# Kernel optimization log

Hardware: AMD Instinct MI355X
Metric: run time of the kernel (lower is better)

## Reference

```python
import jax, jax.numpy as jnp
import numpy as np

NEG_INF = -1e18  # fp32 masking constant used by the original module


def setup_inputs() -> dict:
    key0 = jax.random.key(0)
    kq, kk, kv, km, ke = jax.random.split(key0, 5)
    B, L, H, C = 2, 2048, 16, 64
    query = jax.random.normal(kq, (B, L, H, C), dtype=jnp.float32)
    key = jax.random.normal(kk, (B, L, H, C), dtype=jnp.float32)
    value = jax.random.normal(kv, (B, L, H, C), dtype=jnp.float32)
    mask = jax.random.randint(km, (B, L, L), 0, 2).astype(jnp.bool_)
    edge_scores = jax.random.normal(ke, (1, H, L, L), dtype=jnp.float32)
    return {"query": query, "key": key, "value": value, "mask": mask,
            "edge_scores": edge_scores}


def _masked_softmax(att_score, mask):
    # mask: True -> keep, False -> masked. Fill with -1e18 (fp32 path),
    # softmax, then multiply by mask (post-softmax zeroing), as in original.
    s = jnp.where(mask, att_score, NEG_INF)
    w = jax.nn.softmax(s, axis=-1)
    return w * mask.astype(w.dtype)


def reference(query, key, value, mask, edge_scores):
    # layout 'NTK': query/key/value (B, L, H, C); mask (B, Lq, Lm)
    scale = jnp.sqrt(jnp.asarray(query.shape[-1], dtype=query.dtype))
    # scores: (B, H, Lq, Lm)
    scores = jnp.einsum('binc,bjnc->bnij', query, key)
    scores = scores + edge_scores
    attn_weights = _masked_softmax(scores / scale, mask[:, None, :, :])
    # dropout rate is 0.0 -> identity
    # context: (B, Lq, H, Cv) -> (B, Lq, H*Cv)
    context = jnp.einsum('bnij,bjnc->binc', attn_weights, value)
    B, Lq = context.shape[0], context.shape[1]
    context_vec = context.reshape(B, Lq, -1)
    return (context_vec, scores, attn_weights)
```

## Files before the change

kernel.cpp:

```cpp
#include <hip/hip_runtime.h>


typedef __attribute__((ext_vector_type(8))) short bf16x8;
typedef __attribute__((ext_vector_type(4))) float f32x4;
typedef __attribute__((ext_vector_type(4))) int   i32x4;

#define LQ 2048
#define NH 16
#define CD 64

__device__ inline short f2bf(float x) {
    union { float f; unsigned u; } v; v.f = x;
    unsigned r = v.u + 0x7FFFu + ((v.u >> 16) & 1u);
    return (short)(r >> 16);
}

__device__ inline bf16x8 pack8(f32x4 a, f32x4 b) {
    bf16x8 r;
    r[0] = f2bf(a[0]); r[1] = f2bf(a[1]); r[2] = f2bf(a[2]); r[3] = f2bf(a[3]);
    r[4] = f2bf(b[0]); r[5] = f2bf(b[1]); r[6] = f2bf(b[2]); r[7] = f2bf(b[3]);
    return r;
}

__device__ inline void lds_barrier() {
    asm volatile("s_waitcnt lgkmcnt(0)" ::: "memory");
    __builtin_amdgcn_s_barrier();
}

__global__ __launch_bounds__(256, 4)
void k_attn(const float* __restrict__ q, const float* __restrict__ kk,
            const float* __restrict__ v, const int* __restrict__ mask,
            const float* __restrict__ edge,
            float* __restrict__ sc, float* __restrict__ attn,
            float* __restrict__ ctx)
{
    __shared__ short KsD[2][64][66];
    __shared__ short Vt[64][66];
    __shared__ short Wt[4][16][66];

    const int flat = blockIdx.x;
    const int L = (flat & 7) * 128 + (flat >> 3);
    const int z = L >> 5;
    const int i0 = (L & 31) * 64;
    const int b = z & 1, h = z >> 1;

    const int tid = threadIdx.x;
    const int r = tid >> 2, seg = (tid & 3) * 16;
    const int wave = tid >> 6, lane = tid & 63;
    const int quad = lane >> 4, mm = lane & 15;

    const int gi = i0 + wave * 16 + mm;
    const float* qp = q + ((size_t)((b * LQ + gi) * NH + h)) * CD;
    bf16x8 qa0 = pack8(*(const f32x4*)(qp + quad * 8), *(const f32x4*)(qp + quad * 8 + 4));
    bf16x8 qa1 = pack8(*(const f32x4*)(qp + 32 + quad * 8), *(const f32x4*)(qp + 32 + quad * 8 + 4));

    const float* erow = edge + ((size_t)(h * LQ + gi)) * LQ;
    const int*   mrow = mask + ((size_t)(b * LQ + gi)) * LQ;
    const size_t srow = ((size_t)((b * NH + h) * LQ + gi)) * LQ;

    const float* kbase = kk + ((size_t)((b * LQ + r) * NH + h)) * CD + seg;
    const float* vbase = v  + ((size_t)((b * LQ + r) * NH + h)) * CD + seg;
    const size_t kstep = (size_t)64 * NH * CD;

    f32x4 ev[4]; i32x4 mv[4];
    #pragma unroll
    for (int jt = 0; jt < 4; ++jt) {
        ev[jt] = *(const f32x4*)(erow + jt * 16 + quad * 4);
        mv[jt] = *(const i32x4*)(mrow + jt * 16 + quad * 4);
    }

    f32x4 kr[4];
    #pragma unroll
    for (int u = 0; u < 4; ++u) kr[u] = ((const f32x4*)kbase)[u];
    #pragma unroll
    for (int u = 0; u < 4; ++u)
        *(short4*)&KsD[0][r][seg + u * 4] =
            make_short4(f2bf(kr[u][0]), f2bf(kr[u][1]), f2bf(kr[u][2]), f2bf(kr[u][3]));
    #pragma unroll
    for (int u = 0; u < 4; ++u) kr[u] = ((const f32x4*)(kbase + kstep))[u];
    lds_barrier();

    float lacc = 0.f;
    for (int jb = 0; jb < 32; ++jb) {
        const int j0 = jb * 64;
        const int cur = jb & 1;
        if (jb < 31) {
            #pragma unroll
            for (int u = 0; u < 4; ++u)
                *(short4*)&KsD[cur ^ 1][r][seg + u * 4] =
                    make_short4(f2bf(kr[u][0]), f2bf(kr[u][1]), f2bf(kr[u][2]), f2bf(kr[u][3]));
            if (jb < 30) {
                const float* kp = kbase + kstep * (jb + 2);
                #pragma unroll
                for (int u = 0; u < 4; ++u) kr[u] = ((const f32x4*)kp)[u];
            }
        }
        f32x4 acc[4];
        #pragma unroll
        for (int jt = 0; jt < 4; ++jt) {
            bf16x8 k0 = *(const bf16x8*)&KsD[cur][jt * 16 + mm][quad * 8];
            bf16x8 k1 = *(const bf16x8*)&KsD[cur][jt * 16 + mm][32 + quad * 8];
            f32x4 a = {0.f, 0.f, 0.f, 0.f};
            a = __builtin_amdgcn_mfma_f32_16x16x32_bf16(k0, qa0, a, 0, 0, 0);
            a = __builtin_amdgcn_mfma_f32_16x16x32_bf16(k1, qa1, a, 0, 0, 0);
            acc[jt] = a;
        }
        #pragma unroll
        for (int jt = 0; jt < 4; ++jt) {
            f32x4 s4 = acc[jt] + ev[jt];
            *(f32x4*)(sc + srow + j0 + jt * 16 + quad * 4) = s4;
            lacc += (mv[jt][0] ? __expf(s4[0] * 0.125f) : 0.f)
                  + (mv[jt][1] ? __expf(s4[1] * 0.125f) : 0.f)
                  + (mv[jt][2] ? __expf(s4[2] * 0.125f) : 0.f)
                  + (mv[jt][3] ? __expf(s4[3] * 0.125f) : 0.f);
        }
        if (jb < 31) {
            #pragma unroll
            for (int jt = 0; jt < 4; ++jt) {
                ev[jt] = *(const f32x4*)(erow + j0 + 64 + jt * 16 + quad * 4);
                mv[jt] = *(const i32x4*)(mrow + j0 + 64 + jt * 16 + quad * 4);
            }
        }
        lds_barrier();
    }

    lacc += __shfl_xor(lacc, 16, 64);
    lacc += __shfl_xor(lacc, 32, 64);
    const float inv = (lacc > 0.f) ? 1.f / lacc : 0.f;

    f32x4 vr[4];
    #pragma unroll
    for (int u = 0; u < 4; ++u) { kr[u] = ((const f32x4*)kbase)[u]; vr[u] = ((const f32x4*)vbase)[u]; }
    #pragma unroll
    for (int jt = 0; jt < 4; ++jt) {
        ev[jt] = *(const f32x4*)(erow + jt * 16 + quad * 4);
        mv[jt] = *(const i32x4*)(mrow + jt * 16 + quad * 4);
    }
    f32x4 cacc[4] = { {0,0,0,0}, {0,0,0,0}, {0,0,0,0}, {0,0,0,0} };

    for (int jb = 0; jb < 32; ++jb) {
        const int j0 = jb * 64;
        #pragma unroll
        for (int u = 0; u < 4; ++u) {
            *(short4*)&KsD[0][r][seg + u * 4] =
                make_short4(f2bf(kr[u][0]), f2bf(kr[u][1]), f2bf(kr[u][2]), f2bf(kr[u][3]));
            Vt[seg + u * 4 + 0][r] = f2bf(vr[u][0]);
            Vt[seg + u * 4 + 1][r] = f2bf(vr[u][1]);
            Vt[seg + u * 4 + 2][r] = f2bf(vr[u][2]);
            Vt[seg + u * 4 + 3][r] = f2bf(vr[u][3]);
        }
        lds_barrier();

        f32x4 acc[4];
        #pragma unroll
        for (int jt = 0; jt < 4; ++jt) {
            bf16x8 k0 = *(const bf16x8*)&KsD[0][jt * 16 + mm][quad * 8];
            bf16x8 k1 = *(const bf16x8*)&KsD[0][jt * 16 + mm][32 + quad * 8];
            f32x4 a = {0.f, 0.f, 0.f, 0.f};
            a = __builtin_amdgcn_mfma_f32_16x16x32_bf16(k0, qa0, a, 0, 0, 0);
            a = __builtin_amdgcn_mfma_f32_16x16x32_bf16(k1, qa1, a, 0, 0, 0);
            acc[jt] = a;
        }

        if (jb < 31) {
            const float* kp = kbase + kstep * (jb + 1);
            const float* vp = vbase + kstep * (jb + 1);
            #pragma unroll
            for (int u = 0; u < 4; ++u) { kr[u] = ((const f32x4*)kp)[u]; vr[u] = ((const f32x4*)vp)[u]; }
        }

        #pragma unroll
        for (int jt = 0; jt < 4; ++jt) {
            const int jl = jt * 16 + quad * 4;
            f32x4 s4 = acc[jt] + ev[jt];
            f32x4 w;
            w[0] = mv[jt][0] ? __expf(s4[0] * 0.125f) * inv : 0.f;
            w[1] = mv[jt][1] ? __expf(s4[1] * 0.125f) * inv : 0.f;
            w[2] = mv[jt][2] ? __expf(s4[2] * 0.125f) * inv : 0.f;
            w[3] = mv[jt][3] ? __expf(s4[3] * 0.125f) * inv : 0.f;
            *(f32x4*)(attn + srow + j0 + jl) = w;
            *(short4*)&Wt[wave][mm][jl] = make_short4(f2bf(w[0]), f2bf(w[1]), f2bf(w[2]), f2bf(w[3]));
        }

        if (jb < 31) {
            #pragma unroll
            for (int jt = 0; jt < 4; ++jt) {
                ev[jt] = *(const f32x4*)(erow + j0 + 64 + jt * 16 + quad * 4);
                mv[jt] = *(const i32x4*)(mrow + j0 + 64 + jt * 16 + quad * 4);
            }
        }

        #pragma unroll
        for (int kt = 0; kt < 2; ++kt) {
            bf16x8 aw = *(const bf16x8*)&Wt[wave][mm][kt * 32 + quad * 8];
            #pragma unroll
            for (int nt = 0; nt < 4; ++nt) {
                bf16x8 bb = *(const bf16x8*)&Vt[nt * 16 + mm][kt * 32 + quad * 8];
                cacc[nt] = __builtin_amdgcn_mfma_f32_16x16x32_bf16(aw, bb, cacc[nt], 0, 0, 0);
            }
        }
        lds_barrier();
    }

    const int irow = i0 + wave * 16 + quad * 4;
    #pragma unroll
    for (int nt = 0; nt < 4; ++nt) {
        const int c = nt * 16 + mm;
        #pragma unroll
        for (int reg = 0; reg < 4; ++reg) {
            const int i = irow + reg;
            ctx[((size_t)(b * LQ + i)) * (NH * CD) + h * CD + c] = cacc[nt][reg];
        }
    }
}

extern "C" void kernel_launch(void* const* d_in, const int* in_sizes, int n_in,
                              void* d_out, int out_size, void* d_ws, size_t ws_size,
                              hipStream_t stream) {
    const float* q    = (const float*)d_in[0];
    const float* k    = (const float*)d_in[1];
    const float* v    = (const float*)d_in[2];
    const int*   mask = (const int*)d_in[3];
    const float* edge = (const float*)d_in[4];

    float* out = (float*)d_out;
    float* ctx = out;
    float* sc  = out + 4194304;
    float* at  = sc + 134217728;

    k_attn<<<dim3(1024), 256, 0, stream>>>(q, k, v, mask, edge, sc, at, ctx);
}
```

Before: 1.646 ms.

## Swizzle LDS tiles, vectorize V transpose, use nontemporal output stores

Replaces the padded LDS arrays with XOR-swizzled 128-byte rows so the 16-byte bf16x8 reads stay conflict-free while staying aligned. V is now loaded as four rows per thread, so the transpose into LDS can be written as short4 stores instead of scalar 2-byte stores. Scores, attention weights and context are written with nontemporal stores to avoid polluting cache with the large streaming outputs. The kernel is dominated by roughly 1 GB of score/attn writes plus edge/mask reads, so the LDS changes may matter little.

```diff
diff --git a/kernel.cpp b/kernel.cpp
--- a/kernel.cpp
+++ b/kernel.cpp
@@ -26,6 +26,9 @@
     asm volatile("s_waitcnt lgkmcnt(0)" ::: "memory");
     __builtin_amdgcn_s_barrier();
 }
+
+#define SWZ(base, row, bytecol) \
+    ((char*)(base) + ((row) * 128) + ((bytecol) ^ (((row) & 7) << 4)))
 
 __global__ __launch_bounds__(256, 4)
 void k_attn(const float* __restrict__ q, const float* __restrict__ kk,
@@ -34,9 +37,9 @@
             float* __restrict__ sc, float* __restrict__ attn,
             float* __restrict__ ctx)
 {
-    __shared__ short KsD[2][64][66];
-    __shared__ short Vt[64][66];
-    __shared__ short Wt[4][16][66];
+    __shared__ short KsD[2][64][64];
+    __shared__ short Vt[64][64];
+    __shared__ short Wt[4][16][64];
 
     const int flat = blockIdx.x;
     const int L = (flat & 7) * 128 + (flat >> 3);
@@ -46,8 +49,14 @@
 
     const int tid = threadIdx.x;
     const int r = tid >> 2, seg = (tid & 3) * 16;
+    const int rgrp = tid >> 4, c4 = tid & 15;
     const int wave = tid >> 6, lane = tid & 63;
     const int quad = lane >> 4, mm = lane & 15;
+
+    char* const ks0 = (char*)&KsD[0][0][0];
+    char* const ks1 = (char*)&KsD[1][0][0];
+    char* const vtb = (char*)&Vt[0][0];
+    char* const wtb = (char*)&Wt[wave][0][0];
 
     const int gi = i0 + wave * 16 + mm;
     const float* qp = q + ((size_t)((b * LQ + gi) * NH + h)) * CD;
@@ -59,7 +68,7 @@
     const size_t srow = ((size_t)((b * NH + h) * LQ + gi)) * LQ;
 
     const float* kbase = kk + ((size_t)((b * LQ + r) * NH + h)) * CD + seg;
-    const float* vbase = v  + ((size_t)((b * LQ + r) * NH + h)) * CD + seg;
+    const float* vbase = v  + ((size_t)((b * LQ + rgrp * 4) * NH + h)) * CD + c4 * 4;
     const size_t kstep = (size_t)64 * NH * CD;
 
     f32x4 ev[4]; i32x4 mv[4];
@@ -74,7 +83,7 @@
     for (int u = 0; u < 4; ++u) kr[u] = ((const f32x4*)kbase)[u];
     #pragma unroll
     for (int u = 0; u < 4; ++u)
-        *(short4*)&KsD[0][r][seg + u * 4] =
+        *(short4*)SWZ(ks0, r, 2 * seg + 8 * u) =
             make_short4(f2bf(kr[u][0]), f2bf(kr[u][1]), f2bf(kr[u][2]), f2bf(kr[u][3]));
     #pragma unroll
     for (int u = 0; u < 4; ++u) kr[u] = ((const f32x4*)(kbase + kstep))[u];
@@ -83,11 +92,12 @@
     float lacc = 0.f;
     for (int jb = 0; jb < 32; ++jb) {
         const int j0 = jb * 64;
-        const int cur = jb & 1;
+        char* const kscur = (jb & 1) ? ks1 : ks0;
+        char* const ksnxt = (jb & 1) ? ks0 : ks1;
         if (jb < 31) {
             #pragma unroll
             for (int u = 0; u < 4; ++u)
-                *(short4*)&KsD[cur ^ 1][r][seg + u * 4] =
+                *(short4*)SWZ(ksnxt, r, 2 * seg + 8 * u) =
                     make_short4(f2bf(kr[u][0]), f2bf(kr[u][1]), f2bf(kr[u][2]), f2bf(kr[u][3]));
             if (jb < 30) {
                 const float* kp = kbase + kstep * (jb + 2);
@@ -98,8 +108,8 @@
         f32x4 acc[4];
         #pragma unroll
         for (int jt = 0; jt < 4; ++jt) {
-            bf16x8 k0 = *(const bf16x8*)&KsD[cur][jt * 16 + mm][quad * 8];
-            bf16x8 k1 = *(const bf16x8*)&KsD[cur][jt * 16 + mm][32 + quad * 8];
+            bf16x8 k0 = *(const bf16x8*)SWZ(kscur, jt * 16 + mm, 16 * quad);
+            bf16x8 k1 = *(const bf16x8*)SWZ(kscur, jt * 16 + mm, 64 + 16 * quad);
             f32x4 a = {0.f, 0.f, 0.f, 0.f};
             a = __builtin_amdgcn_mfma_f32_16x16x32_bf16(k0, qa0, a, 0, 0, 0);
             a = __builtin_amdgcn_mfma_f32_16x16x32_bf16(k1, qa1, a, 0, 0, 0);
@@ -108,7 +118,7 @@
         #pragma unroll
         for (int jt = 0; jt < 4; ++jt) {
             f32x4 s4 = acc[jt] + ev[jt];
-            *(f32x4*)(sc + srow + j0 + jt * 16 + quad * 4) = s4;
+            __builtin_nontemporal_store(s4, (f32x4*)(sc + srow + j0 + jt * 16 + quad * 4));
             lacc += (mv[jt][0] ? __expf(s4[0] * 0.125f) : 0.f)
                   + (mv[jt][1] ? __expf(s4[1] * 0.125f) : 0.f)
                   + (mv[jt][2] ? __expf(s4[2] * 0.125f) : 0.f)
@@ -130,7 +140,9 @@
 
     f32x4 vr[4];
     #pragma unroll
-    for (int u = 0; u < 4; ++u) { kr[u] = ((const f32x4*)kbase)[u]; vr[u] = ((const f32x4*)vbase)[u]; }
+    for (int u = 0; u < 4; ++u) kr[u] = ((const f32x4*)kbase)[u];
+    #pragma unroll
+    for (int t = 0; t < 4; ++t) vr[t] = *(const f32x4*)(vbase + t * (NH * CD));
     #pragma unroll
     for (int jt = 0; jt < 4; ++jt) {
         ev[jt] = *(const f32x4*)(erow + jt * 16 + quad * 4);
@@ -141,21 +153,20 @@
     for (int jb = 0; jb < 32; ++jb) {
         const int j0 = jb * 64;
         #pragma unroll
-        for (int u = 0; u < 4; ++u) {
-            *(short4*)&KsD[0][r][seg + u * 4] =
+        for (int u = 0; u < 4; ++u)
+            *(short4*)SWZ(ks0, r, 2 * seg + 8 * u) =
                 make_short4(f2bf(kr[u][0]), f2bf(kr[u][1]), f2bf(kr[u][2]), f2bf(kr[u][3]));
-            Vt[seg + u * 4 + 0][r] = f2bf(vr[u][0]);
-            Vt[seg + u * 4 + 1][r] = f2bf(vr[u][1]);
-            Vt[seg + u * 4 + 2][r] = f2bf(vr[u][2]);
-            Vt[seg + u * 4 + 3][r] = f2bf(vr[u][3]);
-        }
+        #pragma unroll
+        for (int cs = 0; cs < 4; ++cs)
+            *(short4*)SWZ(vtb, c4 * 4 + cs, 8 * rgrp) =
+                make_short4(f2bf(vr[0][cs]), f2bf(vr[1][cs]), f2bf(vr[2][cs]), f2bf(vr[3][cs]));
         lds_barrier();
 
         f32x4 acc[4];
         #pragma unroll
         for (int jt = 0; jt < 4; ++jt) {
-            bf16x8 k0 = *(const bf16x8*)&KsD[0][jt * 16 + mm][quad * 8];
-            bf16x8 k1 = *(const bf16x8*)&KsD[0][jt * 16 + mm][32 + quad * 8];
+            bf16x8 k0 = *(const bf16x8*)SWZ(ks0, jt * 16 + mm, 16 * quad);
+            bf16x8 k1 = *(const bf16x8*)SWZ(ks0, jt * 16 + mm, 64 + 16 * quad);
             f32x4 a = {0.f, 0.f, 0.f, 0.f};
             a = __builtin_amdgcn_mfma_f32_16x16x32_bf16(k0, qa0, a, 0, 0, 0);
             a = __builtin_amdgcn_mfma_f32_16x16x32_bf16(k1, qa1, a, 0, 0, 0);
@@ -166,20 +177,22 @@
             const float* kp = kbase + kstep * (jb + 1);
             const float* vp = vbase + kstep * (jb + 1);
             #pragma unroll
-            for (int u = 0; u < 4; ++u) { kr[u] = ((const f32x4*)kp)[u]; vr[u] = ((const f32x4*)vp)[u]; }
-        }
-
-        #pragma unroll
-        for (int jt = 0; jt < 4; ++jt) {
-            const int jl = jt * 16 + quad * 4;
+            for (int u = 0; u < 4; ++u) kr[u] = ((const f32x4*)kp)[u];
+            #pragma unroll
+            for (int t = 0; t < 4; ++t) vr[t] = *(const f32x4*)(vp + t * (NH * CD));
+        }
+
+        #pragma unroll
+        for (int jt = 0; jt < 4; ++jt) {
             f32x4 s4 = acc[jt] + ev[jt];
             f32x4 w;
             w[0] = mv[jt][0] ? __expf(s4[0] * 0.125f) * inv : 0.f;
             w[1] = mv[jt][1] ? __expf(s4[1] * 0.125f) * inv : 0.f;
             w[2] = mv[jt][2] ? __expf(s4[2] * 0.125f) * inv : 0.f;
             w[3] = mv[jt][3] ? __expf(s4[3] * 0.125f) * inv : 0.f;
-            *(f32x4*)(attn + srow + j0 + jl) = w;
-            *(short4*)&Wt[wave][mm][jl] = make_short4(f2bf(w[0]), f2bf(w[1]), f2bf(w[2]), f2bf(w[3]));
+            __builtin_nontemporal_store(w, (f32x4*)(attn + srow + j0 + jt * 16 + quad * 4));
+            *(short4*)SWZ(wtb, mm, 32 * jt + 8 * quad) =
+                make_short4(f2bf(w[0]), f2bf(w[1]), f2bf(w[2]), f2bf(w[3]));
         }
 
         if (jb < 31) {
@@ -192,10 +205,10 @@
 
         #pragma unroll
         for (int kt = 0; kt < 2; ++kt) {
-            bf16x8 aw = *(const bf16x8*)&Wt[wave][mm][kt * 32 + quad * 8];
+            bf16x8 aw = *(const bf16x8*)SWZ(wtb, mm, 64 * kt + 16 * quad);
             #pragma unroll
             for (int nt = 0; nt < 4; ++nt) {
-                bf16x8 bb = *(const bf16x8*)&Vt[nt * 16 + mm][kt * 32 + quad * 8];
+                bf16x8 bb = *(const bf16x8*)SWZ(vtb, nt * 16 + mm, 64 * kt + 16 * quad);
                 cacc[nt] = __builtin_amdgcn_mfma_f32_16x16x32_bf16(aw, bb, cacc[nt], 0, 0, 0);
             }
         }
@@ -209,7 +222,8 @@
         #pragma unroll
         for (int reg = 0; reg < 4; ++reg) {
             const int i = irow + reg;
-            ctx[((size_t)(b * LQ + i)) * (NH * CD) + h * CD + c] = cacc[nt][reg];
+            __builtin_nontemporal_store(cacc[nt][reg],
+                ctx + ((size_t)(b * LQ + i)) * (NH * CD) + h * CD + c);
         }
     }
 }
```

Measured after the change: 1.672 ms. About the same (+1.5%).

## Share edge-score tiles across both batches per block with swizzled LDS

Applied to the files above, without the earlier changes.

Each block now handles 32 query rows for both batch elements of one head. Two waves per batch share the same edge_scores rows, which should improve cache reuse of the large edge tensor. The padded LDS arrays are replaced with one XOR-swizzled buffer to avoid bank conflicts, and V is loaded in a layout that makes the transpose into LDS use vectorized stores. Mask values are no longer prefetched into registers, the K/V prefetch in the second pass is dropped so those loads are no longer overlapped, and more LDS is used per block.

```diff
diff --git a/kernel.cpp b/kernel.cpp
--- a/kernel.cpp
+++ b/kernel.cpp
@@ -8,6 +8,7 @@
 #define LQ 2048
 #define NH 16
 #define CD 64
+#define NHC (NH*CD)
 
 __device__ inline short f2bf(float x) {
     union { float f; unsigned u; } v; v.f = x;
@@ -26,6 +27,10 @@
     asm volatile("s_waitcnt lgkmcnt(0)" ::: "memory");
     __builtin_amdgcn_s_barrier();
 }
+
+#define SWZ(base, row, bytecol) \
+    ((char*)(base) + ((row) * 128) + ((bytecol) ^ (((row) & 7) << 4)))
+
 
 __global__ __launch_bounds__(256, 4)
 void k_attn(const float* __restrict__ q, const float* __restrict__ kk,
@@ -34,50 +39,58 @@
             float* __restrict__ sc, float* __restrict__ attn,
             float* __restrict__ ctx)
 {
-    __shared__ short KsD[2][64][66];
-    __shared__ short Vt[64][66];
-    __shared__ short Wt[4][16][66];
+    __shared__ __align__(16) char lds[40960];
 
     const int flat = blockIdx.x;
     const int L = (flat & 7) * 128 + (flat >> 3);
-    const int z = L >> 5;
-    const int i0 = (L & 31) * 64;
-    const int b = z & 1, h = z >> 1;
+    const int h = L >> 6;
+    const int i0 = (L & 63) * 32;
 
     const int tid = threadIdx.x;
     const int r = tid >> 2, seg = (tid & 3) * 16;
+    const int rgrp = tid >> 4, c4 = tid & 15;
     const int wave = tid >> 6, lane = tid & 63;
     const int quad = lane >> 4, mm = lane & 15;
-
-    const int gi = i0 + wave * 16 + mm;
-    const float* qp = q + ((size_t)((b * LQ + gi) * NH + h)) * CD;
+    const int wb = wave >> 1;
+    const int wr = wave & 1;
+
+    char* const wtb = lds + 32768 + wave * 2048;
+
+    const int gi = i0 + wr * 16 + mm;
+    const float* qp = q + ((size_t)((wb * LQ + gi) * NH + h)) * CD;
     bf16x8 qa0 = pack8(*(const f32x4*)(qp + quad * 8), *(const f32x4*)(qp + quad * 8 + 4));
     bf16x8 qa1 = pack8(*(const f32x4*)(qp + 32 + quad * 8), *(const f32x4*)(qp + 32 + quad * 8 + 4));
 
     const float* erow = edge + ((size_t)(h * LQ + gi)) * LQ;
-    const int*   mrow = mask + ((size_t)(b * LQ + gi)) * LQ;
-    const size_t srow = ((size_t)((b * NH + h) * LQ + gi)) * LQ;
-
-    const float* kbase = kk + ((size_t)((b * LQ + r) * NH + h)) * CD + seg;
-    const float* vbase = v  + ((size_t)((b * LQ + r) * NH + h)) * CD + seg;
-    const size_t kstep = (size_t)64 * NH * CD;
-
-    f32x4 ev[4]; i32x4 mv[4];
-    #pragma unroll
-    for (int jt = 0; jt < 4; ++jt) {
+    const int*   mrow = mask + ((size_t)(wb * LQ + gi)) * LQ;
+    const size_t srow = ((size_t)((wb * NH + h) * LQ + gi)) * LQ;
+
+    const float* k0p = kk + ((size_t)(r * NH + h)) * CD + seg;
+    const float* k1p = k0p + (size_t)LQ * NHC;
+    const float* v0p = v + ((size_t)((rgrp * 4) * NH + h)) * CD + c4 * 4;
+    const float* v1p = v0p + (size_t)LQ * NHC;
+    const size_t kstep = (size_t)64 * NHC;
+
+    f32x4 ev[4];
+    #pragma unroll
+    for (int jt = 0; jt < 4; ++jt)
         ev[jt] = *(const f32x4*)(erow + jt * 16 + quad * 4);
-        mv[jt] = *(const i32x4*)(mrow + jt * 16 + quad * 4);
-    }
-
-    f32x4 kr[4];
-    #pragma unroll
-    for (int u = 0; u < 4; ++u) kr[u] = ((const f32x4*)kbase)[u];
-    #pragma unroll
-    for (int u = 0; u < 4; ++u)
-        *(short4*)&KsD[0][r][seg + u * 4] =
-            make_short4(f2bf(kr[u][0]), f2bf(kr[u][1]), f2bf(kr[u][2]), f2bf(kr[u][3]));
-    #pragma unroll
-    for (int u = 0; u < 4; ++u) kr[u] = ((const f32x4*)(kbase + kstep))[u];
+
+    f32x4 kr0[4], kr1[4];
+    #pragma unroll
+    for (int u = 0; u < 4; ++u) { kr0[u] = ((const f32x4*)k0p)[u]; kr1[u] = ((const f32x4*)k1p)[u]; }
+    #pragma unroll
+    for (int u = 0; u < 4; ++u) {
+        *(short4*)SWZ(lds, r, 2 * seg + 8 * u) =
+            make_short4(f2bf(kr0[u][0]), f2bf(kr0[u][1]), f2bf(kr0[u][2]), f2bf(kr0[u][3]));
+        *(short4*)SWZ(lds + 8192, r, 2 * seg + 8 * u) =
+            make_short4(f2bf(kr1[u][0]), f2bf(kr1[u][1]), f2bf(kr1[u][2]), f2bf(kr1[u][3]));
+    }
+    #pragma unroll
+    for (int u = 0; u < 4; ++u) {
+        kr0[u] = ((const f32x4*)(k0p + kstep))[u];
+        kr1[u] = ((const f32x4*)(k1p + kstep))[u];
+    }
     lds_barrier();
 
     float lacc = 0.f;
@@ -85,41 +98,47 @@
         const int j0 = jb * 64;
         const int cur = jb & 1;
         if (jb < 31) {
-            #pragma unroll
-            for (int u = 0; u < 4; ++u)
-                *(short4*)&KsD[cur ^ 1][r][seg + u * 4] =
-                    make_short4(f2bf(kr[u][0]), f2bf(kr[u][1]), f2bf(kr[u][2]), f2bf(kr[u][3]));
+            char* kn0 = lds + ((cur ^ 1) * 2) * 8192;
+            char* kn1 = kn0 + 8192;
+            #pragma unroll
+            for (int u = 0; u < 4; ++u) {
+                *(short4*)SWZ(kn0, r, 2 * seg + 8 * u) =
+                    make_short4(f2bf(kr0[u][0]), f2bf(kr0[u][1]), f2bf(kr0[u][2]), f2bf(kr0[u][3]));
+                *(short4*)SWZ(kn1, r, 2 * seg + 8 * u) =
+                    make_short4(f2bf(kr1[u][0]), f2bf(kr1[u][1]), f2bf(kr1[u][2]), f2bf(kr1[u][3]));
+            }
             if (jb < 30) {
-                const float* kp = kbase + kstep * (jb + 2);
+                const float* a0 = k0p + kstep * (jb + 2);
+                const float* a1 = k1p + kstep * (jb + 2);
                 #pragma unroll
-                for (int u = 0; u < 4; ++u) kr[u] = ((const f32x4*)kp)[u];
-            }
-        }
+                for (int u = 0; u < 4; ++u) { kr0[u] = ((const f32x4*)a0)[u]; kr1[u] = ((const f32x4*)a1)[u]; }
+            }
+        }
+        char* const kb = lds + (cur * 2 + wb) * 8192;
         f32x4 acc[4];
         #pragma unroll
         for (int jt = 0; jt < 4; ++jt) {
-            bf16x8 k0 = *(const bf16x8*)&KsD[cur][jt * 16 + mm][quad * 8];
-            bf16x8 k1 = *(const bf16x8*)&KsD[cur][jt * 16 + mm][32 + quad * 8];
+            bf16x8 kf0 = *(const bf16x8*)SWZ(kb, jt * 16 + mm, 16 * quad);
+            bf16x8 kf1 = *(const bf16x8*)SWZ(kb, jt * 16 + mm, 64 + 16 * quad);
             f32x4 a = {0.f, 0.f, 0.f, 0.f};
-            a = __builtin_amdgcn_mfma_f32_16x16x32_bf16(k0, qa0, a, 0, 0, 0);
-            a = __builtin_amdgcn_mfma_f32_16x16x32_bf16(k1, qa1, a, 0, 0, 0);
+            a = __builtin_amdgcn_mfma_f32_16x16x32_bf16(kf0, qa0, a, 0, 0, 0);
+            a = __builtin_amdgcn_mfma_f32_16x16x32_bf16(kf1, qa1, a, 0, 0, 0);
             acc[jt] = a;
         }
         #pragma unroll
         for (int jt = 0; jt < 4; ++jt) {
+            i32x4 m = *(const i32x4*)(mrow + j0 + jt * 16 + quad * 4);
             f32x4 s4 = acc[jt] + ev[jt];
             *(f32x4*)(sc + srow + j0 + jt * 16 + quad * 4) = s4;
-            lacc += (mv[jt][0] ? __expf(s4[0] * 0.125f) : 0.f)
-                  + (mv[jt][1] ? __expf(s4[1] * 0.125f) : 0.f)
-                  + (mv[jt][2] ? __expf(s4[2] * 0.125f) : 0.f)
-                  + (mv[jt][3] ? __expf(s4[3] * 0.125f) : 0.f);
+            lacc += (m[0] ? __expf(s4[0] * 0.125f) : 0.f)
+                  + (m[1] ? __expf(s4[1] * 0.125f) : 0.f)
+                  + (m[2] ? __expf(s4[2] * 0.125f) : 0.f)
+                  + (m[3] ? __expf(s4[3] * 0.125f) : 0.f);
         }
         if (jb < 31) {
             #pragma unroll
-            for (int jt = 0; jt < 4; ++jt) {
+            for (int jt = 0; jt < 4; ++jt)
                 ev[jt] = *(const f32x4*)(erow + j0 + 64 + jt * 16 + quad * 4);
-                mv[jt] = *(const i32x4*)(mrow + j0 + 64 + jt * 16 + quad * 4);
-            }
         }
         lds_barrier();
     }
@@ -128,88 +147,93 @@
     lacc += __shfl_xor(lacc, 32, 64);
     const float inv = (lacc > 0.f) ? 1.f / lacc : 0.f;
 
-    f32x4 vr[4];
-    #pragma unroll
-    for (int u = 0; u < 4; ++u) { kr[u] = ((const f32x4*)kbase)[u]; vr[u] = ((const f32x4*)vbase)[u]; }
-    #pragma unroll
-    for (int jt = 0; jt < 4; ++jt) {
+    #pragma unroll
+    for (int jt = 0; jt < 4; ++jt)
         ev[jt] = *(const f32x4*)(erow + jt * 16 + quad * 4);
-        mv[jt] = *(const i32x4*)(mrow + jt * 16 + quad * 4);
-    }
     f32x4 cacc[4] = { {0,0,0,0}, {0,0,0,0}, {0,0,0,0}, {0,0,0,0} };
 
     for (int jb = 0; jb < 32; ++jb) {
         const int j0 = jb * 64;
-        #pragma unroll
-        for (int u = 0; u < 4; ++u) {
-            *(short4*)&KsD[0][r][seg + u * 4] =
-                make_short4(f2bf(kr[u][0]), f2bf(kr[u][1]), f2bf(kr[u][2]), f2bf(kr[u][3]));
-            Vt[seg + u * 4 + 0][r] = f2bf(vr[u][0]);
-            Vt[seg + u * 4 + 1][r] = f2bf(vr[u][1]);
-            Vt[seg + u * 4 + 2][r] = f2bf(vr[u][2]);
-            Vt[seg + u * 4 + 3][r] = f2bf(vr[u][3]);
+        {
+            const float* a0 = k0p + kstep * jb;
+            const float* a1 = k1p + kstep * jb;
+            const float* b0 = v0p + kstep * jb;
+            const float* b1 = v1p + kstep * jb;
+            f32x4 ka[4], kb4[4], va[4], vb4[4];
+            #pragma unroll
+            for (int u = 0; u < 4; ++u) { ka[u] = ((const f32x4*)a0)[u]; kb4[u] = ((const f32x4*)a1)[u]; }
+            #pragma unroll
+            for (int t = 0; t < 4; ++t) { va[t] = *(const f32x4*)(b0 + t * NHC); vb4[t] = *(const f32x4*)(b1 + t * NHC); }
+            #pragma unroll
+            for (int u = 0; u < 4; ++u) {
+                *(short4*)SWZ(lds, r, 2 * seg + 8 * u) =
+                    make_short4(f2bf(ka[u][0]), f2bf(ka[u][1]), f2bf(ka[u][2]), f2bf(ka[u][3]));
+                *(short4*)SWZ(lds + 8192, r, 2 * seg + 8 * u) =
+                    make_short4(f2bf(kb4[u][0]), f2bf(kb4[u][1]), f2bf(kb4[u][2]), f2bf(kb4[u][3]));
+            }
+            #pragma unroll
+            for (int cs = 0; cs < 4; ++cs) {
+                *(short4*)SWZ(lds + 16384, c4 * 4 + cs, 8 * rgrp) =
+                    make_short4(f2bf(va[0][cs]), f2bf(va[1][cs]), f2bf(va[2][cs]), f2bf(va[3][cs]));
+                *(short4*)SWZ(lds + 24576, c4 * 4 + cs, 8 * rgrp) =
+                    make_short4(f2bf(vb4[0][cs]), f2bf(vb4[1][cs]), f2bf(vb4[2][cs]), f2bf(vb4[3][cs]));
+            }
         }
         lds_barrier();
 
+        char* const kb = lds + wb * 8192;
         f32x4 acc[4];
         #pragma unroll
         for (int jt = 0; jt < 4; ++jt) {
-            bf16x8 k0 = *(const bf16x8*)&KsD[0][jt * 16 + mm][quad * 8];
-            bf16x8 k1 = *(const bf16x8*)&KsD[0][jt * 16 + mm][32 + quad * 8];
+            bf16x8 kf0 = *(const bf16x8*)SWZ(kb, jt * 16 + mm, 16 * quad);
+            bf16x8 kf1 = *(const bf16x8*)SWZ(kb, jt * 16 + mm, 64 + 16 * quad);
             f32x4 a = {0.f, 0.f, 0.f, 0.f};
-            a = __builtin_amdgcn_mfma_f32_16x16x32_bf16(k0, qa0, a, 0, 0, 0);
-            a = __builtin_amdgcn_mfma_f32_16x16x32_bf16(k1, qa1, a, 0, 0, 0);
+            a = __builtin_amdgcn_mfma_f32_16x16x32_bf16(kf0, qa0, a, 0, 0, 0);
+            a = __builtin_amdgcn_mfma_f32_16x16x32_bf16(kf1, qa1, a, 0, 0, 0);
             acc[jt] = a;
         }
 
-        if (jb < 31) {
-            const float* kp = kbase + kstep * (jb + 1);
-            const float* vp = vbase + kstep * (jb + 1);
-            #pragma unroll
-            for (int u = 0; u < 4; ++u) { kr[u] = ((const f32x4*)kp)[u]; vr[u] = ((const f32x4*)vp)[u]; }
-        }
-
-        #pragma unroll
-        for (int jt = 0; jt < 4; ++jt) {
-            const int jl = jt * 16 + quad * 4;
+        #pragma unroll
+        for (int jt = 0; jt < 4; ++jt) {
+            i32x4 m = *(const i32x4*)(mrow + j0 + jt * 16 + quad * 4);
             f32x4 s4 = acc[jt] + ev[jt];
             f32x4 w;
-            w[0] = mv[jt][0] ? __expf(s4[0] * 0.125f) * inv : 0.f;
-            w[1] = mv[jt][1] ? __expf(s4[1] * 0.125f) * inv : 0.f;
-            w[2] = mv[jt][2] ? __expf(s4[2] * 0.125f) * inv : 0.f;
-            w[3] = mv[jt][3] ? __expf(s4[3] * 0.125f) * inv : 0.f;
-            *(f32x4*)(attn + srow + j0 + jl) = w;
-            *(short4*)&Wt[wave][mm][jl] = make_short4(f2bf(w[0]), f2bf(w[1]), f2bf(w[2]), f2bf(w[3]));
+            w[0] = m[0] ? __expf(s4[0] * 0.125f) * inv : 0.f;
+            w[1] = m[1] ? __expf(s4[1] * 0.125f) * inv : 0.f;
+            w[2] = m[2] ? __expf(s4[2] * 0.125f) * inv : 0.f;
+            w[3] = m[3] ? __expf(s4[3] * 0.125f) * inv : 0.f;
+            *(f32x4*)(attn + srow + j0 + jt * 16 + quad * 4) = w;
+            *(short4*)SWZ(wtb, mm, 32 * jt + 8 * quad) =
+                make_short4(f2bf(w[0]), f2bf(w[1]), f2bf(w[2]), f2bf(w[3]));
         }
 
         if (jb < 31) {
             #pragma unroll
-            for (int jt = 0; jt < 4; ++jt) {
+            for (int jt = 0; jt < 4; ++jt)
                 ev[jt] = *(const f32x4*)(erow + j0 + 64 + jt * 16 + quad * 4);
-                mv[jt] = *(const i32x4*)(mrow + j0 + 64 + jt * 16 + quad * 4);
-            }
-        }
-
+        }
+
+        char* const vb = lds + 16384 + wb * 8192;
         #pragma unroll
         for (int kt = 0; kt < 2; ++kt) {
-            bf16x8 aw = *(const bf16x8*)&Wt[wave][mm][kt * 32 + quad * 8];
+            bf16x8 aw = *(const bf16x8*)SWZ(wtb, mm, 64 * kt + 16 * quad);
             #pragma unroll
             for (int nt = 0; nt < 4; ++nt) {
-                bf16x8 bb = *(const bf16x8*)&Vt[nt * 16 + mm][kt * 32 + quad * 8];
-                cacc[nt] = __builtin_amdgcn_mfma_f32_16x16x32_bf16(aw, bb, cacc[nt], 0, 0, 0);
+                bf16x8 bbv = *(const bf16x8*)SWZ(vb, nt * 16 + mm, 64 * kt + 16 * quad);
+                cacc[nt] = __builtin_amdgcn_mfma_f32_16x16x32_bf16(aw, bbv, cacc[nt], 0, 0, 0);
             }
         }
         lds_barrier();
     }
 
-    const int irow = i0 + wave * 16 + quad * 4;
+    const int irow = i0 + wr * 16 + quad * 4;
     #pragma unroll
     for (int nt = 0; nt < 4; ++nt) {
         const int c = nt * 16 + mm;
         #pragma unroll
         for (int reg = 0; reg < 4; ++reg) {
             const int i = irow + reg;
-            ctx[((size_t)(b * LQ + i)) * (NH * CD) + h * CD + c] = cacc[nt][reg];
+            ctx[((size_t)(wb * LQ + i)) * NHC + h * CD + c] = cacc[nt][reg];
         }
     }
 }
```

New measurement: 1.843 ms. +11.9%, slower.

## Share edge-score tiles across both batches in one block via LDS

Applied to the files above, without the earlier changes.

Each block now handles both batch items for one head and query tile: 512 threads, 8 waves, with each half of the block handling one batch. The edge_scores tile, which is the same for both batches, is loaded once into double-buffered LDS and shared, so its global reads are halved. K, V and the weight tiles move to an XOR-swizzled LDS layout to avoid bank conflicts. The cost is a larger LDS footprint per block and half as many blocks, which may reduce occupancy.

```diff
diff --git a/kernel.cpp b/kernel.cpp
--- a/kernel.cpp
+++ b/kernel.cpp
@@ -8,6 +8,7 @@
 #define LQ 2048
 #define NH 16
 #define CD 64
+#define NHC (NH*CD)
 
 __device__ inline short f2bf(float x) {
     union { float f; unsigned u; } v; v.f = x;
@@ -27,57 +28,73 @@
     __builtin_amdgcn_s_barrier();
 }
 
-__global__ __launch_bounds__(256, 4)
+#define SWZ(base, row, bytecol) \
+    ((char*)(base) + ((row) * 128) + ((bytecol) ^ (((row) & 7) << 4)))
+
+#define EDGE_LDS(s) (lds + 32768 + (s) * 17408)
+#define EDGE_AT(base, row, colf32) ((float*)(base) + (row) * 68 + (colf32))
+
+__global__ __launch_bounds__(512, 4)
 void k_attn(const float* __restrict__ q, const float* __restrict__ kk,
             const float* __restrict__ v, const int* __restrict__ mask,
             const float* __restrict__ edge,
             float* __restrict__ sc, float* __restrict__ attn,
             float* __restrict__ ctx)
 {
-    __shared__ short KsD[2][64][66];
-    __shared__ short Vt[64][66];
-    __shared__ short Wt[4][16][66];
+    __shared__ __align__(16) char lds[67584];
 
     const int flat = blockIdx.x;
-    const int L = (flat & 7) * 128 + (flat >> 3);
-    const int z = L >> 5;
+    const int L = (flat & 7) * 64 + (flat >> 3);
+    const int h = L >> 5;
     const int i0 = (L & 31) * 64;
-    const int b = z & 1, h = z >> 1;
 
     const int tid = threadIdx.x;
-    const int r = tid >> 2, seg = (tid & 3) * 16;
+    const int bb = tid >> 8;
+    const int tt = tid & 255;
+    const int r = tt >> 2, seg = (tt & 3) * 16;
+    const int erow_st = tid >> 3, ecol_st = (tid & 7) * 8;
     const int wave = tid >> 6, lane = tid & 63;
     const int quad = lane >> 4, mm = lane & 15;
-
-    const int gi = i0 + wave * 16 + mm;
-    const float* qp = q + ((size_t)((b * LQ + gi) * NH + h)) * CD;
+    const int wb = wave >> 2;
+    const int wrow = wave & 3;
+
+    char* const wtb = lds + 50176 + wave * 2048;
+
+    const int gi = i0 + wrow * 16 + mm;
+    const float* qp = q + ((size_t)((wb * LQ + gi) * NH + h)) * CD;
     bf16x8 qa0 = pack8(*(const f32x4*)(qp + quad * 8), *(const f32x4*)(qp + quad * 8 + 4));
     bf16x8 qa1 = pack8(*(const f32x4*)(qp + 32 + quad * 8), *(const f32x4*)(qp + 32 + quad * 8 + 4));
 
-    const float* erow = edge + ((size_t)(h * LQ + gi)) * LQ;
-    const int*   mrow = mask + ((size_t)(b * LQ + gi)) * LQ;
-    const size_t srow = ((size_t)((b * NH + h) * LQ + gi)) * LQ;
-
-    const float* kbase = kk + ((size_t)((b * LQ + r) * NH + h)) * CD + seg;
-    const float* vbase = v  + ((size_t)((b * LQ + r) * NH + h)) * CD + seg;
-    const size_t kstep = (size_t)64 * NH * CD;
-
-    f32x4 ev[4]; i32x4 mv[4];
-    #pragma unroll
-    for (int jt = 0; jt < 4; ++jt) {
-        ev[jt] = *(const f32x4*)(erow + jt * 16 + quad * 4);
+    const int*   mrow = mask + ((size_t)(wb * LQ + gi)) * LQ;
+    const size_t srow = ((size_t)((wb * NH + h) * LQ + gi)) * LQ;
+
+    const float* kst = kk + (size_t)bb * LQ * NHC + ((size_t)(r * NH + h)) * CD + seg;
+    const float* vst = v  + (size_t)bb * LQ * NHC + ((size_t)(r * NH + h)) * CD + seg;
+    const float* est = edge + ((size_t)(h * LQ + i0 + erow_st)) * LQ + ecol_st;
+    const size_t kstep = (size_t)64 * NHC;
+
+    f32x4 kr[4], er0, er1;
+    #pragma unroll
+    for (int u = 0; u < 4; ++u) kr[u] = ((const f32x4*)kst)[u];
+    er0 = *(const f32x4*)est; er1 = *(const f32x4*)(est + 4);
+    {
+        char* kb = lds + bb * 8192;
+        #pragma unroll
+        for (int u = 0; u < 4; ++u)
+            *(short4*)SWZ(kb, r, 2 * seg + 8 * u) =
+                make_short4(f2bf(kr[u][0]), f2bf(kr[u][1]), f2bf(kr[u][2]), f2bf(kr[u][3]));
+        *(f32x4*)EDGE_AT(EDGE_LDS(0), erow_st, ecol_st) = er0;
+        *(f32x4*)EDGE_AT(EDGE_LDS(0), erow_st, ecol_st + 4) = er1;
+    }
+    #pragma unroll
+    for (int u = 0; u < 4; ++u) kr[u] = ((const f32x4*)(kst + kstep))[u];
+    er0 = *(const f32x4*)(est + 64); er1 = *(const f32x4*)(est + 68);
+
+    i32x4 mv[4];
+    #pragma unroll
+    for (int jt = 0; jt < 4; ++jt)
         mv[jt] = *(const i32x4*)(mrow + jt * 16 + quad * 4);
-    }
-
-    f32x4 kr[4];
-    #pragma unroll
-    for (int u = 0; u < 4; ++u) kr[u] = ((const f32x4*)kbase)[u];
-    #pragma unroll
-    for (int u = 0; u < 4; ++u)
-        *(short4*)&KsD[0][r][seg + u * 4] =
-            make_short4(f2bf(kr[u][0]), f2bf(kr[u][1]), f2bf(kr[u][2]), f2bf(kr[u][3]));
-    #pragma unroll
-    for (int u = 0; u < 4; ++u) kr[u] = ((const f32x4*)(kbase + kstep))[u];
+
     lds_barrier();
 
     float lacc = 0.f;
@@ -85,29 +102,37 @@
         const int j0 = jb * 64;
         const int cur = jb & 1;
         if (jb < 31) {
+            char* kn = lds + ((cur ^ 1) * 2 + bb) * 8192;
             #pragma unroll
             for (int u = 0; u < 4; ++u)
-                *(short4*)&KsD[cur ^ 1][r][seg + u * 4] =
+                *(short4*)SWZ(kn, r, 2 * seg + 8 * u) =
                     make_short4(f2bf(kr[u][0]), f2bf(kr[u][1]), f2bf(kr[u][2]), f2bf(kr[u][3]));
+            *(f32x4*)EDGE_AT(EDGE_LDS(cur ^ 1), erow_st, ecol_st) = er0;
+            *(f32x4*)EDGE_AT(EDGE_LDS(cur ^ 1), erow_st, ecol_st + 4) = er1;
             if (jb < 30) {
-                const float* kp = kbase + kstep * (jb + 2);
+                const float* kp = kst + kstep * (jb + 2);
                 #pragma unroll
                 for (int u = 0; u < 4; ++u) kr[u] = ((const f32x4*)kp)[u];
+                er0 = *(const f32x4*)(est + (size_t)(jb + 2) * 64);
+                er1 = *(const f32x4*)(est + (size_t)(jb + 2) * 64 + 4);
             }
         }
+        char* const kb = lds + (cur * 2 + wb) * 8192;
         f32x4 acc[4];
         #pragma unroll
         for (int jt = 0; jt < 4; ++jt) {
-            bf16x8 k0 = *(const bf16x8*)&KsD[cur][jt * 16 + mm][quad * 8];
-            bf16x8 k1 = *(const bf16x8*)&KsD[cur][jt * 16 + mm][32 + quad * 8];
+            bf16x8 kf0 = *(const bf16x8*)SWZ(kb, jt * 16 + mm, 16 * quad);
+            bf16x8 kf1 = *(const bf16x8*)SWZ(kb, jt * 16 + mm, 64 + 16 * quad);
             f32x4 a = {0.f, 0.f, 0.f, 0.f};
-            a = __builtin_amdgcn_mfma_f32_16x16x32_bf16(k0, qa0, a, 0, 0, 0);
-            a = __builtin_amdgcn_mfma_f32_16x16x32_bf16(k1, qa1, a, 0, 0, 0);
+            a = __builtin_amdgcn_mfma_f32_16x16x32_bf16(kf0, qa0, a, 0, 0, 0);
+            a = __builtin_amdgcn_mfma_f32_16x16x32_bf16(kf1, qa1, a, 0, 0, 0);
             acc[jt] = a;
         }
-        #pragma unroll
-        for (int jt = 0; jt < 4; ++jt) {
-            f32x4 s4 = acc[jt] + ev[jt];
+        char* const eb = EDGE_LDS(cur);
+        #pragma unroll
+        for (int jt = 0; jt < 4; ++jt) {
+            f32x4 ev = *(const f32x4*)EDGE_AT(eb, wrow * 16 + mm, jt * 16 + quad * 4);
+            f32x4 s4 = acc[jt] + ev;
             *(f32x4*)(sc + srow + j0 + jt * 16 + quad * 4) = s4;
             lacc += (mv[jt][0] ? __expf(s4[0] * 0.125f) : 0.f)
                   + (mv[jt][1] ? __expf(s4[1] * 0.125f) : 0.f)
@@ -116,10 +141,8 @@
         }
         if (jb < 31) {
             #pragma unroll
-            for (int jt = 0; jt < 4; ++jt) {
-                ev[jt] = *(const f32x4*)(erow + j0 + 64 + jt * 16 + quad * 4);
+            for (int jt = 0; jt < 4; ++jt)
                 mv[jt] = *(const i32x4*)(mrow + j0 + 64 + jt * 16 + quad * 4);
-            }
         }
         lds_barrier();
     }
@@ -130,86 +153,96 @@
 
     f32x4 vr[4];
     #pragma unroll
-    for (int u = 0; u < 4; ++u) { kr[u] = ((const f32x4*)kbase)[u]; vr[u] = ((const f32x4*)vbase)[u]; }
-    #pragma unroll
-    for (int jt = 0; jt < 4; ++jt) {
-        ev[jt] = *(const f32x4*)(erow + jt * 16 + quad * 4);
+    for (int u = 0; u < 4; ++u) { kr[u] = ((const f32x4*)kst)[u]; vr[u] = ((const f32x4*)vst)[u]; }
+    er0 = *(const f32x4*)est; er1 = *(const f32x4*)(est + 4);
+    #pragma unroll
+    for (int jt = 0; jt < 4; ++jt)
         mv[jt] = *(const i32x4*)(mrow + jt * 16 + quad * 4);
-    }
+
     f32x4 cacc[4] = { {0,0,0,0}, {0,0,0,0}, {0,0,0,0}, {0,0,0,0} };
 
     for (int jb = 0; jb < 32; ++jb) {
         const int j0 = jb * 64;
-        #pragma unroll
-        for (int u = 0; u < 4; ++u) {
-            *(short4*)&KsD[0][r][seg + u * 4] =
-                make_short4(f2bf(kr[u][0]), f2bf(kr[u][1]), f2bf(kr[u][2]), f2bf(kr[u][3]));
-            Vt[seg + u * 4 + 0][r] = f2bf(vr[u][0]);
-            Vt[seg + u * 4 + 1][r] = f2bf(vr[u][1]);
-            Vt[seg + u * 4 + 2][r] = f2bf(vr[u][2]);
-            Vt[seg + u * 4 + 3][r] = f2bf(vr[u][3]);
+        {
+            char* kb = lds + bb * 8192;
+            char* vb = lds + 16384 + bb * 8192;
+            #pragma unroll
+            for (int u = 0; u < 4; ++u) {
+                *(short4*)SWZ(kb, r, 2 * seg + 8 * u) =
+                    make_short4(f2bf(kr[u][0]), f2bf(kr[u][1]), f2bf(kr[u][2]), f2bf(kr[u][3]));
+                *(short*)SWZ(vb, seg + u * 4 + 0, r * 2) = f2bf(vr[u][0]);
+                *(short*)SWZ(vb, seg + u * 4 + 1, r * 2) = f2bf(vr[u][1]);
+                *(short*)SWZ(vb, seg + u * 4 + 2, r * 2) = f2bf(vr[u][2]);
+                *(short*)SWZ(vb, seg + u * 4 + 3, r * 2) = f2bf(vr[u][3]);
+            }
+            *(f32x4*)EDGE_AT(EDGE_LDS(0), erow_st, ecol_st) = er0;
+            *(f32x4*)EDGE_AT(EDGE_LDS(0), erow_st, ecol_st + 4) = er1;
         }
         lds_barrier();
 
+        char* const kb = lds + wb * 8192;
         f32x4 acc[4];
         #pragma unroll
         for (int jt = 0; jt < 4; ++jt) {
-            bf16x8 k0 = *(const bf16x8*)&KsD[0][jt * 16 + mm][quad * 8];
-            bf16x8 k1 = *(const bf16x8*)&KsD[0][jt * 16 + mm][32 + quad * 8];
+            bf16x8 kf0 = *(const bf16x8*)SWZ(kb, jt * 16 + mm, 16 * quad);
+            bf16x8 kf1 = *(const bf16x8*)SWZ(kb, jt * 16 + mm, 64 + 16 * quad);
             f32x4 a = {0.f, 0.f, 0.f, 0.f};
-            a = __builtin_amdgcn_mfma_f32_16x16x32_bf16(k0, qa0, a, 0, 0, 0);
-            a = __builtin_amdgcn_mfma_f32_16x16x32_bf16(k1, qa1, a, 0, 0, 0);
+            a = __builtin_amdgcn_mfma_f32_16x16x32_bf16(kf0, qa0, a, 0, 0, 0);
+            a = __builtin_amdgcn_mfma_f32_16x16x32_bf16(kf1, qa1, a, 0, 0, 0);
             acc[jt] = a;
         }
 
         if (jb < 31) {
-            const float* kp = kbase + kstep * (jb + 1);
-            const float* vp = vbase + kstep * (jb + 1);
+            const float* kp = kst + kstep * (jb + 1);
+            const float* vp = vst + kstep * (jb + 1);
             #pragma unroll
             for (int u = 0; u < 4; ++u) { kr[u] = ((const f32x4*)kp)[u]; vr[u] = ((const f32x4*)vp)[u]; }
-        }
-
-        #pragma unroll
-        for (int jt = 0; jt < 4; ++jt) {
-            const int jl = jt * 16 + quad * 4;
-            f32x4 s4 = acc[jt] + ev[jt];
+            er0 = *(const f32x4*)(est + (size_t)(jb + 1) * 64);
+            er1 = *(const f32x4*)(est + (size_t)(jb + 1) * 64 + 4);
+        }
+
+        char* const eb = EDGE_LDS(0);
+        #pragma unroll
+        for (int jt = 0; jt < 4; ++jt) {
+            f32x4 ev = *(const f32x4*)EDGE_AT(eb, wrow * 16 + mm, jt * 16 + quad * 4);
+            f32x4 s4 = acc[jt] + ev;
             f32x4 w;
             w[0] = mv[jt][0] ? __expf(s4[0] * 0.125f) * inv : 0.f;
             w[1] = mv[jt][1] ? __expf(s4[1] * 0.125f) * inv : 0.f;
             w[2] = mv[jt][2] ? __expf(s4[2] * 0.125f) * inv : 0.f;
             w[3] = mv[jt][3] ? __expf(s4[3] * 0.125f) * inv : 0.f;
-            *(f32x4*)(attn + srow + j0 + jl) = w;
-            *(short4*)&Wt[wave][mm][jl] = make_short4(f2bf(w[0]), f2bf(w[1]), f2bf(w[2]), f2bf(w[3]));
-        }
-
-        if (jb < 31) {
-            #pragma unroll
-            for (int jt = 0; jt < 4; ++jt) {
-                ev[jt] = *(const f32x4*)(erow + j0 + 64 + jt * 16 + quad * 4);
+            *(f32x4*)(attn + srow + j0 + jt * 16 + quad * 4) = w;
+            *(short4*)SWZ(wtb, mm, 32 * jt + 8 * quad) =
+                make_short4(f2bf(w[0]), f2bf(w[1]), f2bf(w[2]), f2bf(w[3]));
+        }
+
+        if (jb < 31) {
+            #pragma unroll
+            for (int jt = 0; jt < 4; ++jt)
                 mv[jt] = *(const i32x4*)(mrow + j0 + 64 + jt * 16 + quad * 4);
+        }
+
+        char* const vb = lds + 16384 + wb * 8192;
+        #pragma unroll
+        for (int kt = 0; kt < 2; ++kt) {
+            bf16x8 aw = *(const bf16x8*)SWZ(wtb, mm, 64 * kt + 16 * quad);
+            #pragma unroll
+            for (int nt = 0; nt < 4; ++nt) {
+                bf16x8 bbv = *(const bf16x8*)SWZ(vb, nt * 16 + mm, 64 * kt + 16 * quad);
+                cacc[nt] = __builtin_amdgcn_mfma_f32_16x16x32_bf16(aw, bbv, cacc[nt], 0, 0, 0);
             }
         }
-
-        #pragma unroll
-        for (int kt = 0; kt < 2; ++kt) {
-            bf16x8 aw = *(const bf16x8*)&Wt[wave][mm][kt * 32 + quad * 8];
-            #pragma unroll
-            for (int nt = 0; nt < 4; ++nt) {
-                bf16x8 bb = *(const bf16x8*)&Vt[nt * 16 + mm][kt * 32 + quad * 8];
-                cacc[nt] = __builtin_amdgcn_mfma_f32_16x16x32_bf16(aw, bb, cacc[nt], 0, 0, 0);
-            }
-        }
         lds_barrier();
     }
 
-    const int irow = i0 + wave * 16 + quad * 4;
+    const int irow = i0 + wrow * 16 + quad * 4;
     #pragma unroll
     for (int nt = 0; nt < 4; ++nt) {
         const int c = nt * 16 + mm;
         #pragma unroll
         for (int reg = 0; reg < 4; ++reg) {
             const int i = irow + reg;
-            ctx[((size_t)(b * LQ + i)) * (NH * CD) + h * CD + c] = cacc[nt][reg];
+            ctx[((size_t)(wb * LQ + i)) * NHC + h * CD + c] = cacc[nt][reg];
         }
     }
 }
@@ -228,5 +261,5 @@
     float* sc  = out + 4194304;
     float* at  = sc + 134217728;
 
-    k_attn<<<dim3(1024), 256, 0, stream>>>(q, k, v, mask, edge, sc, at, ctx);
-}
+    k_attn<<<dim3(512), 512, 0, stream>>>(q, k, v, mask, edge, sc, at, ctx);
+}
```

New measurement: 1.672 ms. No clear change (+1.5%).
